# Kernel optimization log

Measured on AMD Instinct MI355X. Metric: run time of the kernel, lower is better.

## Reference

```python
import jax, jax.numpy as jnp
import numpy as np

NODE_SIZE = 50000
REL_SIZE = 2000
TRIPLE_SIZE = 1000000
HID = 128
DEPTH = 2


def _rows_covering(key, n_rows, n_seg):
    # sorted row indices guaranteeing every segment appears at least once
    extra = jax.random.randint(key, (n_rows - n_seg,), 0, n_seg)
    return jnp.sort(jnp.concatenate([jnp.arange(n_seg), extra])).astype(jnp.int32)


def setup_inputs() -> dict:
    key = jax.random.key(0)
    ks = jax.random.split(key, 12)
    adj = jnp.stack([_rows_covering(ks[0], TRIPLE_SIZE, NODE_SIZE),
                     jax.random.randint(ks[1], (TRIPLE_SIZE,), 0, NODE_SIZE, dtype=jnp.int32)])
    r_index = jnp.stack([jnp.arange(TRIPLE_SIZE, dtype=jnp.int32),
                         jax.random.randint(ks[2], (TRIPLE_SIZE,), 0, REL_SIZE, dtype=jnp.int32)])
    r_val = jax.random.uniform(ks[3], (TRIPLE_SIZE,), dtype=jnp.float32)
    ent_adj = jnp.stack([_rows_covering(ks[4], TRIPLE_SIZE, NODE_SIZE),
                         jax.random.randint(ks[5], (TRIPLE_SIZE,), 0, NODE_SIZE, dtype=jnp.int32)])
    rel_adj = jnp.stack([_rows_covering(ks[6], TRIPLE_SIZE, NODE_SIZE),
                         jax.random.randint(ks[7], (TRIPLE_SIZE,), 0, REL_SIZE, dtype=jnp.int32)])
    ent_emb = jax.random.normal(ks[8], (NODE_SIZE, HID), dtype=jnp.float32) * 0.05
    rel_emb = jax.random.normal(ks[9], (REL_SIZE, HID), dtype=jnp.float32) * 0.05
    attn_e = jax.random.normal(ks[10], (DEPTH, HID, 1), dtype=jnp.float32) * 0.1
    attn_r = jax.random.normal(ks[11], (DEPTH, HID, 1), dtype=jnp.float32) * 0.1
    return {"ent_emb": ent_emb, "rel_emb": rel_emb, "attn_e": attn_e, "attn_r": attn_r,
            "adj": adj, "r_index": r_index, "r_val": r_val,
            "ent_adj": ent_adj, "rel_adj": rel_adj}


def _avg(adj, emb, node_size):
    # sparse softmax over all-ones values == mean over neighbors
    rows, cols = adj[0], adj[1]
    deg = jax.ops.segment_sum(jnp.ones_like(rows, dtype=emb.dtype), rows, node_size)
    s = jax.ops.segment_sum(emb[cols], rows, node_size)  # [node_size, d]
    return s / jnp.maximum(deg, 1.0)[:, None]


def _segment_softmax(vals, seg, num_seg):
    m = jax.ops.segment_max(vals, seg, num_seg)
    e = jnp.exp(vals - m[seg])
    s = jax.ops.segment_sum(e, seg, num_seg)
    return e / s[seg]


def _nr_graph_attention(features, rel_emb, adj, r_index, r_val, attn_kernels):
    feats = jnp.tanh(features)
    outs = [feats]
    src, dst = adj[0], adj[1]
    for l in range(DEPTH):
        # sparse [T, R] @ rel_emb -> per-triple relation vector
        tri_rel = jax.ops.segment_sum(r_val[:, None] * rel_emb[r_index[1]], r_index[0], TRIPLE_SIZE)
        tri_rel = tri_rel / jnp.maximum(jnp.linalg.norm(tri_rel, axis=1, keepdims=True), 1e-12)
        neighs = feats[dst]  # [T, H]
        # Householder reflection of neighbor feature about tri_rel
        neighs = neighs - 2.0 * jnp.sum(neighs * tri_rel, axis=1, keepdims=True) * tri_rel
        att = jnp.squeeze(tri_rel @ attn_kernels[l], axis=-1)  # [T]
        a = _segment_softmax(att, src, NODE_SIZE)
        feats = jnp.tanh(jax.ops.segment_sum(neighs * a[:, None], src, NODE_SIZE))
        outs.append(feats)
    return jnp.concatenate(outs, axis=-1)  # [N, H*(DEPTH+1)]


def reference(ent_emb, rel_emb, attn_e, attn_r, adj, r_index, r_val, ent_adj, rel_adj):
    ent_feature = _avg(ent_adj, ent_emb, NODE_SIZE)  # [N, H]
    rel_feature = _avg(rel_adj, rel_emb, NODE_SIZE)  # [N, H]
    out_rel = _nr_graph_attention(rel_feature, rel_emb, adj, r_index, r_val, attn_r)
    out_ent = _nr_graph_attention(ent_feature, rel_emb, adj, r_index, r_val, attn_e)
    return jnp.concatenate([out_ent, out_rel], axis=-1)  # dropout rate 0 -> identity
```

## Files before the change

### kernel.cpp

```cpp
#include <hip/hip_runtime.h>
#include <hip/hip_fp16.h>
#include <math.h>

#define NN 50000
#define NR 2000
#define NT 1000000
#define HID 128
#define OSTRIDE 768
#define CH 256

typedef float f32x4 __attribute__((ext_vector_type(4)));
typedef unsigned u32x4 __attribute__((ext_vector_type(4)));
typedef unsigned u32x2 __attribute__((ext_vector_type(2)));

__device__ __forceinline__ float wsum64(float v) {
#pragma unroll
  for (int off = 32; off > 0; off >>= 1) v += __shfl_xor(v, off, 64);
  return v;
}
__device__ __forceinline__ unsigned pack2(float x, float y) {
  __half2 h = __floats2half2_rn(x, y);
  union { __half2 h; unsigned u; } c; c.h = h; return c.u;
}
__device__ __forceinline__ float2 unpack2(unsigned u) {
  union { unsigned u; __half2 h; } c; c.u = u;
  return __half22float2(c.h);
}
__device__ __forceinline__ void nt_store4(const float4& v, float* p) {
  f32x4 t = {v.x, v.y, v.z, v.w};
  __builtin_nontemporal_store(t, (f32x4*)p);
}

__global__ void rowptr3_kernel(const int* __restrict__ a0, int* __restrict__ r0,
                               const int* __restrict__ a1, int* __restrict__ r1,
                               const int* __restrict__ a2, int* __restrict__ r2) {
  const int* rows = (blockIdx.y == 0) ? a0 : (blockIdx.y == 1) ? a1 : a2;
  int* rp = (blockIdx.y == 0) ? r0 : (blockIdx.y == 1) ? r1 : r2;
  int i = blockIdx.x * blockDim.x + threadIdx.x;
  int stride = gridDim.x * blockDim.x;
  for (int t = i; t < NT; t += stride) {
    if (t == 0 || rows[t] != rows[t - 1]) rp[rows[t]] = t;
  }
  if (i == 0) rp[NN] = NT;
}

__global__ __launch_bounds__(256) void relpre_kernel(
    const float* __restrict__ rel_emb, const float* __restrict__ attn_e,
    const float* __restrict__ attn_r, float4* __restrict__ e4,
    float4* __restrict__ tab0, float4* __restrict__ tab1) {
  int wid = (blockIdx.x * blockDim.x + threadIdx.x) >> 6;
  int lane = threadIdx.x & 63;
  if (wid >= NR) return;
  const float2* e2 = (const float2*)rel_emb;
  float2 e = e2[(size_t)wid * 64 + lane];
  float p = wsum64(e.x * e.x + e.y * e.y);
  float inv_n = rsqrtf(p);
  float n2i = 1.f / p;
  const float* ks[4] = {attn_e, attn_e + HID, attn_r, attn_r + HID};
  float d[4];
#pragma unroll
  for (int j = 0; j < 4; ++j) {
    float2 a = ((const float2*)ks[j])[lane];
    d[j] = wsum64(e.x * a.x + e.y * a.y);
  }
  if (lane == 0) {
    float4 ex = make_float4(expf(d[0] * inv_n), expf(d[1] * inv_n),
                            expf(d[2] * inv_n), expf(d[3] * inv_n));
    e4[wid] = ex;
    tab0[wid] = make_float4(ex.x, ex.z, n2i, 0.f);
    tab1[wid] = make_float4(ex.y, ex.w, n2i, 0.f);
  }
}

__global__ __launch_bounds__(256) void cvt_kernel(const float* __restrict__ ent,
                                                  const float* __restrict__ rel,
                                                  __half* __restrict__ enth,
                                                  __half* __restrict__ relh) {
  int i = blockIdx.x * blockDim.x + threadIdx.x;
  const int entu = NN * 16;
  const float4* s4;
  u32x4* d;
  int j;
  if (i < entu) {
    s4 = (const float4*)ent; d = (u32x4*)enth; j = i;
  } else {
    j = i - entu;
    if (j >= NR * 16) return;
    s4 = (const float4*)rel; d = (u32x4*)relh;
  }
  float4 a = s4[2 * j], b = s4[2 * j + 1];
  u32x4 w;
  w.x = pack2(a.x, a.y); w.y = pack2(a.z, a.w);
  w.z = pack2(b.x, b.y); w.w = pack2(b.z, b.w);
  __builtin_nontemporal_store(w, d + j);
}

__global__ __launch_bounds__(256) void avg_tanh_kernel(
    const int* __restrict__ rp_ent, const int* __restrict__ cols_ent,
    const int* __restrict__ rp_rel, const int* __restrict__ cols_rel,
    const __half* __restrict__ enth, const __half* __restrict__ relh,
    float* __restrict__ out, __half* __restrict__ c0h) {
  int wid = (blockIdx.x * blockDim.x + threadIdx.x) >> 6;
  int lane = threadIdx.x & 63;
  if (wid >= NN) return;
  int br = (wid >= NN / 2) ? 1 : 0;
  int pair = wid - br * (NN / 2);
  int node = pair * 2 + (lane >> 5);
  int sl = lane & 31;
  const int* rp = br ? rp_rel : rp_ent;
  const int* cols = br ? cols_rel : cols_ent;
  const u32x2* eb = (const u32x2*)(br ? relh : enth);
  int t0 = rp[node], t1 = rp[node + 1];
  int nmax = t1 - 1;

  int c0 = cols[t0];
  int c1 = cols[min(t0 + 1, nmax)];
  int c2 = cols[min(t0 + 2, nmax)];
  int c3 = cols[min(t0 + 3, nmax)];
  u32x2 h0 = eb[(size_t)c0 * 32 + sl];
  u32x2 h1 = eb[(size_t)c1 * 32 + sl];
  u32x2 h2 = eb[(size_t)c2 * 32 + sl];
  u32x2 h3 = eb[(size_t)c3 * 32 + sl];
  int d0 = cols[min(t0 + 4, nmax)];
  int d1 = cols[min(t0 + 5, nmax)];
  int d2 = cols[min(t0 + 6, nmax)];
  int d3 = cols[min(t0 + 7, nmax)];

  float4 acc = make_float4(0.f, 0.f, 0.f, 0.f);
  for (int t = t0; t < t1; t += 4) {
    u32x2 g0 = eb[(size_t)d0 * 32 + sl];
    u32x2 g1 = eb[(size_t)d1 * 32 + sl];
    u32x2 g2 = eb[(size_t)d2 * 32 + sl];
    u32x2 g3 = eb[(size_t)d3 * 32 + sl];
    int tm = t + 8;
    int n0 = cols[min(tm, nmax)];
    int n1 = cols[min(tm + 1, nmax)];
    int n2 = cols[min(tm + 2, nmax)];
    int n3 = cols[min(tm + 3, nmax)];
    float m1 = (t + 1 < t1) ? 1.f : 0.f;
    float m2 = (t + 2 < t1) ? 1.f : 0.f;
    float m3 = (t + 3 < t1) ? 1.f : 0.f;
    float2 a0 = unpack2(h0.x), b0v = unpack2(h0.y);
    float2 a1 = unpack2(h1.x), b1v = unpack2(h1.y);
    float2 a2 = unpack2(h2.x), b2v = unpack2(h2.y);
    float2 a3 = unpack2(h3.x), b3v = unpack2(h3.y);
    acc.x += a0.x + m1 * a1.x + m2 * a2.x + m3 * a3.x;
    acc.y += a0.y + m1 * a1.y + m2 * a2.y + m3 * a3.y;
    acc.z += b0v.x + m1 * b1v.x + m2 * b2v.x + m3 * b3v.x;
    acc.w += b0v.y + m1 * b1v.y + m2 * b2v.y + m3 * b3v.y;
    h0 = g0; h1 = g1; h2 = g2; h3 = g3;
    d0 = n0; d1 = n1; d2 = n2; d3 = n3;
  }
  float inv = 1.f / (float)(t1 - t0);
  float4 o;
  o.x = tanhf(acc.x * inv); o.y = tanhf(acc.y * inv);
  o.z = tanhf(acc.z * inv); o.w = tanhf(acc.w * inv);
  nt_store4(o, out + (size_t)node * OSTRIDE + (br ? 3 * HID : 0) + sl * 4);
  u32x2 w; w.x = pack2(o.x, o.y); w.y = pack2(o.z, o.w);
  __builtin_nontemporal_store(w, (u32x2*)(c0h + (size_t)node * CH + br * HID + sl * 4));
}

struct BlkT { int dn; int r; float tx, ty, n2i; };

__device__ __forceinline__ BlkT ldblk(int tb, int g, int t1,
                                      const int* __restrict__ dst,
                                      const int* __restrict__ rel_id,
                                      const float* __restrict__ r_val,
                                      const float4* __restrict__ tab) {
  int t = tb + g;
  bool valid = (t < t1);
  int tc = valid ? t : (t1 - 1);
  BlkT b;
  b.dn = dst[tc];
  b.r = rel_id[tc];
  float rv = r_val[tc];
  float4 tv = tab[b.r];
  if (rv <= 0.f) tv = make_float4(1.f, 1.f, 0.f, 0.f);
  b.tx = valid ? tv.x : 0.f;
  b.ty = valid ? tv.y : 0.f;
  b.n2i = tv.z;
  return b;
}

__device__ __forceinline__ float dot8(const float4& a, const float4& b,
                                      const float4& c, const float4& d) {
  return a.x * c.x + a.y * c.y + a.z * c.z + a.w * c.w +
         b.x * d.x + b.y * d.y + b.z * d.z + b.w * d.w;
}
__device__ __forceinline__ void fma_acc(float4& a, float w, const float4& nb,
                                        float c, const float4& u) {
  a.x += w * nb.x + c * u.x;
  a.y += w * nb.y + c * u.y;
  a.z += w * nb.z + c * u.z;
  a.w += w * nb.w + c * u.w;
}
__device__ __forceinline__ float4 comb4(float4 a) {
  a.x += __shfl_xor(a.x, 16, 64); a.y += __shfl_xor(a.y, 16, 64);
  a.z += __shfl_xor(a.z, 16, 64); a.w += __shfl_xor(a.w, 16, 64);
  a.x += __shfl_xor(a.x, 32, 64); a.y += __shfl_xor(a.y, 32, 64);
  a.z += __shfl_xor(a.z, 32, 64); a.w += __shfl_xor(a.w, 32, 64);
  return a;
}

__global__ __launch_bounds__(256) void attn_kernel(
    float* __restrict__ out, const int* __restrict__ rp,
    const int* __restrict__ dst, const int* __restrict__ rel_id,
    const float* __restrict__ r_val, const float* __restrict__ rel_emb,
    const float4* __restrict__ tab, const float4* __restrict__ e4,
    float4* __restrict__ Sinv4, const __half* __restrict__ chin,
    __half* __restrict__ chout, int layer) {
  int wid = (blockIdx.x * blockDim.x + threadIdx.x) >> 6;
  int lane = threadIdx.x & 63;
  if (wid >= NN) return;
  int g = lane >> 4;
  int sl = lane & 15;
  int t0 = rp[wid], t1 = rp[wid + 1];

  float sie, sir;
  if (layer == 0) {
    float4 s = make_float4(0.f, 0.f, 0.f, 0.f);
    for (int t = t0 + lane; t < t1; t += 64) {
      int r = rel_id[t];
      float rv = r_val[t];
      float4 ex = e4[r];
      if (rv <= 0.f) ex = make_float4(1.f, 1.f, 1.f, 1.f);
      s.x += ex.x; s.y += ex.y; s.z += ex.z; s.w += ex.w;
    }
    s.x = wsum64(s.x); s.y = wsum64(s.y); s.z = wsum64(s.z); s.w = wsum64(s.w);
    float4 inv = make_float4(1.f / s.x, 1.f / s.y, 1.f / s.z, 1.f / s.w);
    if (lane == 0) Sinv4[wid] = inv;
    sie = inv.x; sir = inv.z;
  } else {
    float4 sv = Sinv4[wid];
    sie = sv.y; sir = sv.w;
  }

  BlkT b0 = ldblk(t0, g, t1, dst, rel_id, r_val, tab);
  const float4* up = (const float4*)(rel_emb + b0.r * HID + sl * 8);
  float4 u0 = up[0], u1 = up[1];
  const u32x4* ph = (const u32x4*)(chin + (size_t)b0.dn * CH);
  u32x4 eh = ph[sl], qh = ph[16 + sl];
  BlkT b1 = ldblk(t0 + 4, g, t1, dst, rel_id, r_val, tab);

  float4 ae0 = make_float4(0, 0, 0, 0), ae1 = ae0, ar0 = ae0, ar1 = ae0;

  for (int tb = t0; tb < t1; tb += 4) {
    const float4* upN = (const float4*)(rel_emb + b1.r * HID + sl * 8);
    float4 u0N = upN[0], u1N = upN[1];
    const u32x4* phN = (const u32x4*)(chin + (size_t)b1.dn * CH);
    u32x4 ehN = phN[sl], qhN = phN[16 + sl];
    BlkT b2 = ldblk(tb + 8, g, t1, dst, rel_id, r_val, tab);

    float2 p0 = unpack2(eh.x), p1 = unpack2(eh.y);
    float2 p2 = unpack2(eh.z), p3 = unpack2(eh.w);
    float4 e0 = make_float4(p0.x, p0.y, p1.x, p1.y);
    float4 e1 = make_float4(p2.x, p2.y, p3.x, p3.y);
    float2 r0v = unpack2(qh.x), r1v = unpack2(qh.y);
    float2 r2v = unpack2(qh.z), r3v = unpack2(qh.w);
    float4 q0 = make_float4(r0v.x, r0v.y, r1v.x, r1v.y);
    float4 q1 = make_float4(r2v.x, r2v.y, r3v.x, r3v.y);

    float de = dot8(u0, u1, e0, e1);
    float dr = dot8(u0, u1, q0, q1);
#pragma unroll
    for (int off = 1; off < 16; off <<= 1) {
      de += __shfl_xor(de, off, 64);
      dr += __shfl_xor(dr, off, 64);
    }
    float we = b0.tx * sie;
    float wr = b0.ty * sir;
    float ce = -2.f * we * b0.n2i * de;
    float cr = -2.f * wr * b0.n2i * dr;
    fma_acc(ae0, we, e0, ce, u0);
    fma_acc(ae1, we, e1, ce, u1);
    fma_acc(ar0, wr, q0, cr, u0);
    fma_acc(ar1, wr, q1, cr, u1);

    b0 = b1; b1 = b2;
    u0 = u0N; u1 = u1N; eh = ehN; qh = qhN;
  }

  ae0 = comb4(ae0); ae1 = comb4(ae1); ar0 = comb4(ar0); ar1 = comb4(ar1);

  float4 v;
  if (g == 0) v = ae0;
  else if (g == 1) v = ae1;
  else if (g == 2) v = ar0;
  else v = ar1;
  v.x = tanhf(v.x); v.y = tanhf(v.y); v.z = tanhf(v.z); v.w = tanhf(v.w);
  float* ob = (g < 2) ? (out + (size_t)wid * OSTRIDE + (layer + 1) * HID)
                      : (out + (size_t)wid * OSTRIDE + (4 + layer) * HID);
  nt_store4(v, ob + sl * 8 + (g & 1) * 4);
  if (chout) {
    u32x2 w; w.x = pack2(v.x, v.y); w.y = pack2(v.z, v.w);
    __builtin_nontemporal_store(
        w, (u32x2*)(chout + (size_t)wid * CH + (g >> 1) * 128 + sl * 8 + (g & 1) * 4));
  }
}

extern "C" void kernel_launch(void* const* d_in, const int* in_sizes, int n_in,
                              void* d_out, int out_size, void* d_ws, size_t ws_size,
                              hipStream_t stream) {
  const float* ent_emb = (const float*)d_in[0];
  const float* rel_emb = (const float*)d_in[1];
  const float* attn_e = (const float*)d_in[2];
  const float* attn_r = (const float*)d_in[3];
  const int* adj = (const int*)d_in[4];
  const int* r_index = (const int*)d_in[5];
  const float* r_val = (const float*)d_in[6];
  const int* ent_adj = (const int*)d_in[7];
  const int* rel_adj = (const int*)d_in[8];
  float* out = (float*)d_out;

  char* ws = (char*)d_ws;
  __half* enth = (__half*)ws;  ws += (size_t)NN * HID * sizeof(__half);
  __half* relh = (__half*)ws;  ws += (size_t)NR * HID * sizeof(__half);
  __half* C0h = (__half*)ws;   ws += (size_t)NN * CH * sizeof(__half);
  __half* C1h = (__half*)ws;   ws += (size_t)NN * CH * sizeof(__half);
  float4* e4 = (float4*)ws;    ws += (size_t)NR * sizeof(float4);
  float4* tab0 = (float4*)ws;  ws += (size_t)NR * sizeof(float4);
  float4* tab1 = (float4*)ws;  ws += (size_t)NR * sizeof(float4);
  float4* Sinv4 = (float4*)ws; ws += (size_t)NN * sizeof(float4);
  int* rp_adj = (int*)ws;      ws += (NN + 1) * sizeof(int);
  int* rp_ent = (int*)ws;      ws += (NN + 1) * sizeof(int);
  int* rp_rel = (int*)ws;      ws += (NN + 1) * sizeof(int);

  dim3 rg(512, 3);
  rowptr3_kernel<<<rg, 256, 0, stream>>>(adj, rp_adj, ent_adj, rp_ent, rel_adj, rp_rel);
  relpre_kernel<<<(NR * 64) / 256, 256, 0, stream>>>(rel_emb, attn_e, attn_r,
                                                     e4, tab0, tab1);
  cvt_kernel<<<((NN + NR) * 16) / 256, 256, 0, stream>>>(ent_emb, rel_emb, enth, relh);
  avg_tanh_kernel<<<(NN * 64) / 256, 256, 0, stream>>>(
      rp_ent, ent_adj + NT, rp_rel, rel_adj + NT, enth, relh, out, C0h);
  for (int l = 0; l < 2; ++l) {
    attn_kernel<<<(NN * 64) / 256, 256, 0, stream>>>(
        out, rp_adj, adj + NT, r_index + NT, r_val, rel_emb,
        (l == 0) ? tab0 : tab1, e4, Sinv4, (l == 0) ? C0h : C1h,
        (l == 0) ? C1h : nullptr, l);
  }
}
```

Before: 487.0 us.

## Precompute packed per-triple softmax weights and use fp16 relation embeddings in attention

Adds a pre-pass kernel that computes per-node softmax normalisers for both layers. It writes a packed 32-bit (dst, rel) index and fp16-packed weight/Householder coefficients per triple, so each attention layer reads 12 bytes per triple instead of re-gathering rel_id, r_val, a table entry and Sinv. The attention kernel now gathers fp16 relation rows instead of fp32 and uses fdot2 for the dot products. The software prefetch of the next gathered rows is dropped, leaving only the record prefetch. The change adds extra fp16 rounding of weights and embeddings, an extra pass over all triples with about 20MB of writes, and index packing that depends on node and relation ids fitting in 16 bits.

Result: faster. 468.5 us (-3.8%).

```diff
diff --git a/kernel.cpp b/kernel.cpp
--- a/kernel.cpp
+++ b/kernel.cpp
@@ -12,6 +12,10 @@
 typedef float f32x4 __attribute__((ext_vector_type(4)));
 typedef unsigned u32x4 __attribute__((ext_vector_type(4)));
 typedef unsigned u32x2 __attribute__((ext_vector_type(2)));
+typedef _Float16 h16x2 __attribute__((ext_vector_type(2)));
+typedef _Float16 h16x8 __attribute__((ext_vector_type(8)));
+
+union U4H8 { u32x4 u; h16x8 h; };
 
 __device__ __forceinline__ float wsum64(float v) {
 #pragma unroll
@@ -47,7 +51,7 @@
 __global__ __launch_bounds__(256) void relpre_kernel(
     const float* __restrict__ rel_emb, const float* __restrict__ attn_e,
     const float* __restrict__ attn_r, float4* __restrict__ e4,
-    float4* __restrict__ tab0, float4* __restrict__ tab1) {
+    float* __restrict__ n2i_arr) {
   int wid = (blockIdx.x * blockDim.x + threadIdx.x) >> 6;
   int lane = threadIdx.x & 63;
   if (wid >= NR) return;
@@ -55,7 +59,6 @@
   float2 e = e2[(size_t)wid * 64 + lane];
   float p = wsum64(e.x * e.x + e.y * e.y);
   float inv_n = rsqrtf(p);
-  float n2i = 1.f / p;
   const float* ks[4] = {attn_e, attn_e + HID, attn_r, attn_r + HID};
   float d[4];
 #pragma unroll
@@ -64,11 +67,9 @@
     d[j] = wsum64(e.x * a.x + e.y * a.y);
   }
   if (lane == 0) {
-    float4 ex = make_float4(expf(d[0] * inv_n), expf(d[1] * inv_n),
-                            expf(d[2] * inv_n), expf(d[3] * inv_n));
-    e4[wid] = ex;
-    tab0[wid] = make_float4(ex.x, ex.z, n2i, 0.f);
-    tab1[wid] = make_float4(ex.y, ex.w, n2i, 0.f);
+    e4[wid] = make_float4(expf(d[0] * inv_n), expf(d[1] * inv_n),
+                          expf(d[2] * inv_n), expf(d[3] * inv_n));
+    n2i_arr[wid] = 1.f / p;
   }
 }
 
@@ -93,6 +94,44 @@
   w.x = pack2(a.x, a.y); w.y = pack2(a.z, a.w);
   w.z = pack2(b.x, b.y); w.w = pack2(b.z, b.w);
   __builtin_nontemporal_store(w, d + j);
+}
+
+__global__ __launch_bounds__(256) void wpre2_kernel(
+    const int* __restrict__ rp, const int* __restrict__ dst,
+    const int* __restrict__ rel_id, const float* __restrict__ r_val,
+    const float4* __restrict__ e4, const float* __restrict__ n2i_arr,
+    unsigned* __restrict__ pk, u32x2* __restrict__ wq0,
+    u32x2* __restrict__ wq1) {
+  int wid = (blockIdx.x * blockDim.x + threadIdx.x) >> 6;
+  int lane = threadIdx.x & 63;
+  if (wid >= NN) return;
+  int t0 = rp[wid], t1 = rp[wid + 1];
+  float4 s = make_float4(0.f, 0.f, 0.f, 0.f);
+  for (int t = t0 + lane; t < t1; t += 64) {
+    int r = rel_id[t];
+    float rv = r_val[t];
+    float4 ex = e4[r];
+    if (rv <= 0.f) ex = make_float4(1.f, 1.f, 1.f, 1.f);
+    s.x += ex.x; s.y += ex.y; s.z += ex.z; s.w += ex.w;
+  }
+  s.x = wsum64(s.x); s.y = wsum64(s.y); s.z = wsum64(s.z); s.w = wsum64(s.w);
+  float4 inv = make_float4(1.f / s.x, 1.f / s.y, 1.f / s.z, 1.f / s.w);
+  for (int t = t0 + lane; t < t1; t += 64) {
+    int r = rel_id[t];
+    float rv = r_val[t];
+    int dn = dst[t];
+    float4 ex = e4[r];
+    float zi = n2i_arr[r];
+    if (rv <= 0.f) { ex = make_float4(1.f, 1.f, 1.f, 1.f); zi = 0.f; }
+    float we0 = ex.x * inv.x, wr0 = ex.z * inv.z;
+    float we1 = ex.y * inv.y, wr1 = ex.w * inv.w;
+    __builtin_nontemporal_store((unsigned)dn | ((unsigned)r << 16), pk + t);
+    u32x2 a, b;
+    a.x = pack2(we0, wr0); a.y = pack2(-2.f * we0 * zi, -2.f * wr0 * zi);
+    b.x = pack2(we1, wr1); b.y = pack2(-2.f * we1 * zi, -2.f * wr1 * zi);
+    __builtin_nontemporal_store(a, wq0 + t);
+    __builtin_nontemporal_store(b, wq1 + t);
+  }
 }
 
 __global__ __launch_bounds__(256) void avg_tanh_kernel(
@@ -160,54 +199,31 @@
   __builtin_nontemporal_store(w, (u32x2*)(c0h + (size_t)node * CH + br * HID + sl * 4));
 }
 
-struct BlkT { int dn; int r; float tx, ty, n2i; };
-
-__device__ __forceinline__ BlkT ldblk(int tb, int g, int t1,
-                                      const int* __restrict__ dst,
-                                      const int* __restrict__ rel_id,
-                                      const float* __restrict__ r_val,
-                                      const float4* __restrict__ tab) {
-  int t = tb + g;
+struct RecT { int dn; int r; float we, wr, ce, cr; };
+
+__device__ __forceinline__ RecT ldrec(int t, int t1,
+                                      const unsigned* __restrict__ pk,
+                                      const u32x2* __restrict__ wq) {
   bool valid = (t < t1);
   int tc = valid ? t : (t1 - 1);
-  BlkT b;
-  b.dn = dst[tc];
-  b.r = rel_id[tc];
-  float rv = r_val[tc];
-  float4 tv = tab[b.r];
-  if (rv <= 0.f) tv = make_float4(1.f, 1.f, 0.f, 0.f);
-  b.tx = valid ? tv.x : 0.f;
-  b.ty = valid ? tv.y : 0.f;
-  b.n2i = tv.z;
-  return b;
-}
-
-__device__ __forceinline__ float dot8(const float4& a, const float4& b,
-                                      const float4& c, const float4& d) {
-  return a.x * c.x + a.y * c.y + a.z * c.z + a.w * c.w +
-         b.x * d.x + b.y * d.y + b.z * d.z + b.w * d.w;
-}
-__device__ __forceinline__ void fma_acc(float4& a, float w, const float4& nb,
-                                        float c, const float4& u) {
-  a.x += w * nb.x + c * u.x;
-  a.y += w * nb.y + c * u.y;
-  a.z += w * nb.z + c * u.z;
-  a.w += w * nb.w + c * u.w;
-}
-__device__ __forceinline__ float4 comb4(float4 a) {
-  a.x += __shfl_xor(a.x, 16, 64); a.y += __shfl_xor(a.y, 16, 64);
-  a.z += __shfl_xor(a.z, 16, 64); a.w += __shfl_xor(a.w, 16, 64);
-  a.x += __shfl_xor(a.x, 32, 64); a.y += __shfl_xor(a.y, 32, 64);
-  a.z += __shfl_xor(a.z, 32, 64); a.w += __shfl_xor(a.w, 32, 64);
-  return a;
+  unsigned p = pk[tc];
+  u32x2 w = wq[tc];
+  RecT rec;
+  rec.dn = (int)(p & 0xFFFFu);
+  rec.r = (int)(p >> 16);
+  float2 a = unpack2(w.x);
+  float2 b = unpack2(w.y);
+  rec.we = valid ? a.x : 0.f;
+  rec.wr = valid ? a.y : 0.f;
+  rec.ce = valid ? b.x : 0.f;
+  rec.cr = valid ? b.y : 0.f;
+  return rec;
 }
 
 __global__ __launch_bounds__(256) void attn_kernel(
     float* __restrict__ out, const int* __restrict__ rp,
-    const int* __restrict__ dst, const int* __restrict__ rel_id,
-    const float* __restrict__ r_val, const float* __restrict__ rel_emb,
-    const float4* __restrict__ tab, const float4* __restrict__ e4,
-    float4* __restrict__ Sinv4, const __half* __restrict__ chin,
+    const unsigned* __restrict__ pk, const u32x2* __restrict__ wq,
+    const __half* __restrict__ relh, const __half* __restrict__ chin,
     __half* __restrict__ chout, int layer) {
   int wid = (blockIdx.x * blockDim.x + threadIdx.x) >> 6;
   int lane = threadIdx.x & 63;
@@ -216,77 +232,66 @@
   int sl = lane & 15;
   int t0 = rp[wid], t1 = rp[wid + 1];
 
-  float sie, sir;
-  if (layer == 0) {
-    float4 s = make_float4(0.f, 0.f, 0.f, 0.f);
-    for (int t = t0 + lane; t < t1; t += 64) {
-      int r = rel_id[t];
-      float rv = r_val[t];
-      float4 ex = e4[r];
-      if (rv <= 0.f) ex = make_float4(1.f, 1.f, 1.f, 1.f);
-      s.x += ex.x; s.y += ex.y; s.z += ex.z; s.w += ex.w;
+  const u32x4* relh4 = (const u32x4*)relh;
+  RecT b0 = ldrec(t0 + g, t1, pk, wq);
+  float aE[8], aR[8];
+#pragma unroll
+  for (int i = 0; i < 8; ++i) { aE[i] = 0.f; aR[i] = 0.f; }
+
+  for (int tb = t0; tb < t1; tb += 4) {
+    U4H8 uh, eh, qh;
+    uh.u = relh4[(size_t)b0.r * 16 + sl];
+    const u32x4* ph = (const u32x4*)chin + (size_t)b0.dn * 32;
+    eh.u = ph[sl];
+    qh.u = ph[16 + sl];
+    RecT b1 = ldrec(tb + 4 + g, t1, pk, wq);
+
+    float de = 0.f, dr = 0.f;
+#if __has_builtin(__builtin_amdgcn_fdot2)
+#pragma unroll
+    for (int i = 0; i < 4; ++i) {
+      h16x2 up = {uh.h[2 * i], uh.h[2 * i + 1]};
+      h16x2 ep = {eh.h[2 * i], eh.h[2 * i + 1]};
+      h16x2 qp = {qh.h[2 * i], qh.h[2 * i + 1]};
+      de = __builtin_amdgcn_fdot2(up, ep, de, false);
+      dr = __builtin_amdgcn_fdot2(up, qp, dr, false);
     }
-    s.x = wsum64(s.x); s.y = wsum64(s.y); s.z = wsum64(s.z); s.w = wsum64(s.w);
-    float4 inv = make_float4(1.f / s.x, 1.f / s.y, 1.f / s.z, 1.f / s.w);
-    if (lane == 0) Sinv4[wid] = inv;
-    sie = inv.x; sir = inv.z;
-  } else {
-    float4 sv = Sinv4[wid];
-    sie = sv.y; sir = sv.w;
-  }
-
-  BlkT b0 = ldblk(t0, g, t1, dst, rel_id, r_val, tab);
-  const float4* up = (const float4*)(rel_emb + b0.r * HID + sl * 8);
-  float4 u0 = up[0], u1 = up[1];
-  const u32x4* ph = (const u32x4*)(chin + (size_t)b0.dn * CH);
-  u32x4 eh = ph[sl], qh = ph[16 + sl];
-  BlkT b1 = ldblk(t0 + 4, g, t1, dst, rel_id, r_val, tab);
-
-  float4 ae0 = make_float4(0, 0, 0, 0), ae1 = ae0, ar0 = ae0, ar1 = ae0;
-
-  for (int tb = t0; tb < t1; tb += 4) {
-    const float4* upN = (const float4*)(rel_emb + b1.r * HID + sl * 8);
-    float4 u0N = upN[0], u1N = upN[1];
-    const u32x4* phN = (const u32x4*)(chin + (size_t)b1.dn * CH);
-    u32x4 ehN = phN[sl], qhN = phN[16 + sl];
-    BlkT b2 = ldblk(tb + 8, g, t1, dst, rel_id, r_val, tab);
-
-    float2 p0 = unpack2(eh.x), p1 = unpack2(eh.y);
-    float2 p2 = unpack2(eh.z), p3 = unpack2(eh.w);
-    float4 e0 = make_float4(p0.x, p0.y, p1.x, p1.y);
-    float4 e1 = make_float4(p2.x, p2.y, p3.x, p3.y);
-    float2 r0v = unpack2(qh.x), r1v = unpack2(qh.y);
-    float2 r2v = unpack2(qh.z), r3v = unpack2(qh.w);
-    float4 q0 = make_float4(r0v.x, r0v.y, r1v.x, r1v.y);
-    float4 q1 = make_float4(r2v.x, r2v.y, r3v.x, r3v.y);
-
-    float de = dot8(u0, u1, e0, e1);
-    float dr = dot8(u0, u1, q0, q1);
+#else
+#pragma unroll
+    for (int i = 0; i < 8; ++i) {
+      de += (float)uh.h[i] * (float)eh.h[i];
+      dr += (float)uh.h[i] * (float)qh.h[i];
+    }
+#endif
 #pragma unroll
     for (int off = 1; off < 16; off <<= 1) {
       de += __shfl_xor(de, off, 64);
       dr += __shfl_xor(dr, off, 64);
     }
-    float we = b0.tx * sie;
-    float wr = b0.ty * sir;
-    float ce = -2.f * we * b0.n2i * de;
-    float cr = -2.f * wr * b0.n2i * dr;
-    fma_acc(ae0, we, e0, ce, u0);
-    fma_acc(ae1, we, e1, ce, u1);
-    fma_acc(ar0, wr, q0, cr, u0);
-    fma_acc(ar1, wr, q1, cr, u1);
-
-    b0 = b1; b1 = b2;
-    u0 = u0N; u1 = u1N; eh = ehN; qh = qhN;
-  }
-
-  ae0 = comb4(ae0); ae1 = comb4(ae1); ar0 = comb4(ar0); ar1 = comb4(ar1);
+    float ce = b0.ce * de;
+    float cr = b0.cr * dr;
+#pragma unroll
+    for (int i = 0; i < 8; ++i) {
+      float uf = (float)uh.h[i];
+      aE[i] += b0.we * (float)eh.h[i] + ce * uf;
+      aR[i] += b0.wr * (float)qh.h[i] + cr * uf;
+    }
+    b0 = b1;
+  }
+
+#pragma unroll
+  for (int i = 0; i < 8; ++i) {
+    aE[i] += __shfl_xor(aE[i], 16, 64);
+    aE[i] += __shfl_xor(aE[i], 32, 64);
+    aR[i] += __shfl_xor(aR[i], 16, 64);
+    aR[i] += __shfl_xor(aR[i], 32, 64);
+  }
 
   float4 v;
-  if (g == 0) v = ae0;
-  else if (g == 1) v = ae1;
-  else if (g == 2) v = ar0;
-  else v = ar1;
+  if (g == 0) v = make_float4(aE[0], aE[1], aE[2], aE[3]);
+  else if (g == 1) v = make_float4(aE[4], aE[5], aE[6], aE[7]);
+  else if (g == 2) v = make_float4(aR[0], aR[1], aR[2], aR[3]);
+  else v = make_float4(aR[4], aR[5], aR[6], aR[7]);
   v.x = tanhf(v.x); v.y = tanhf(v.y); v.z = tanhf(v.z); v.w = tanhf(v.w);
   float* ob = (g < 2) ? (out + (size_t)wid * OSTRIDE + (layer + 1) * HID)
                       : (out + (size_t)wid * OSTRIDE + (4 + layer) * HID);
@@ -317,25 +322,26 @@
   __half* relh = (__half*)ws;  ws += (size_t)NR * HID * sizeof(__half);
   __half* C0h = (__half*)ws;   ws += (size_t)NN * CH * sizeof(__half);
   __half* C1h = (__half*)ws;   ws += (size_t)NN * CH * sizeof(__half);
+  unsigned* pk = (unsigned*)ws; ws += (size_t)NT * sizeof(unsigned);
+  u32x2* wq0 = (u32x2*)ws;     ws += (size_t)NT * sizeof(u32x2);
+  u32x2* wq1 = (u32x2*)ws;     ws += (size_t)NT * sizeof(u32x2);
   float4* e4 = (float4*)ws;    ws += (size_t)NR * sizeof(float4);
-  float4* tab0 = (float4*)ws;  ws += (size_t)NR * sizeof(float4);
-  float4* tab1 = (float4*)ws;  ws += (size_t)NR * sizeof(float4);
-  float4* Sinv4 = (float4*)ws; ws += (size_t)NN * sizeof(float4);
+  float* n2i = (float*)ws;     ws += (size_t)NR * sizeof(float);
   int* rp_adj = (int*)ws;      ws += (NN + 1) * sizeof(int);
   int* rp_ent = (int*)ws;      ws += (NN + 1) * sizeof(int);
   int* rp_rel = (int*)ws;      ws += (NN + 1) * sizeof(int);
 
   dim3 rg(512, 3);
   rowptr3_kernel<<<rg, 256, 0, stream>>>(adj, rp_adj, ent_adj, rp_ent, rel_adj, rp_rel);
-  relpre_kernel<<<(NR * 64) / 256, 256, 0, stream>>>(rel_emb, attn_e, attn_r,
-                                                     e4, tab0, tab1);
+  relpre_kernel<<<(NR * 64) / 256, 256, 0, stream>>>(rel_emb, attn_e, attn_r, e4, n2i);
   cvt_kernel<<<((NN + NR) * 16) / 256, 256, 0, stream>>>(ent_emb, rel_emb, enth, relh);
+  wpre2_kernel<<<(NN * 64) / 256, 256, 0, stream>>>(
+      rp_adj, adj + NT, r_index + NT, r_val, e4, n2i, pk, wq0, wq1);
   avg_tanh_kernel<<<(NN * 64) / 256, 256, 0, stream>>>(
       rp_ent, ent_adj + NT, rp_rel, rel_adj + NT, enth, relh, out, C0h);
   for (int l = 0; l < 2; ++l) {
     attn_kernel<<<(NN * 64) / 256, 256, 0, stream>>>(
-        out, rp_adj, adj + NT, r_index + NT, r_val, rel_emb,
-        (l == 0) ? tab0 : tab1, e4, Sinv4, (l == 0) ? C0h : C1h,
-        (l == 0) ? C1h : nullptr, l);
-  }
-}
+        out, rp_adj, pk, (l == 0) ? wq0 : wq1, relh,
+        (l == 0) ? C0h : C1h, (l == 0) ? C1h : nullptr, l);
+  }
+}
```
